# Performance work log

Measured on AMD Instinct MI355X. Metric: run time of the kernel, lower is better.

Reference implementation:

```python
import jax, jax.numpy as jnp
import numpy as np

A = 32      # num_agents (nodes per batch element)
B = 256     # batch size
T = 5       # temporal_window_size
H, C = 4, 64  # attention heads, hidden_dim per head
D = H * C   # feature_dim = 256
NEG_SLOPE = 0.2
LATENT = 128
NBS = 64    # num_belief_states
FIN = NBS + 16  # node_feat_dim = num_belief_states + action_dim


def _xavier(k, shape):
    std = (2.0 / (shape[0] + shape[-1])) ** 0.5
    return std * jax.random.normal(k, shape, dtype=jnp.float32)


def setup_inputs() -> dict:
    key = jax.random.key(0)
    ks = jax.random.split(key, 24)
    N = B * A
    # fully-connected directed graph (no self loops) inside each batch block
    ii, jj = np.meshgrid(np.arange(A), np.arange(A), indexing='ij')
    m = ii != jj
    off = (np.arange(B) * A)[:, None]
    src = (off + ii[m][None, :]).ravel()
    dst = (off + jj[m][None, :]).ravel()
    edge_index = jnp.asarray(np.stack([src, dst]), dtype=jnp.int32)  # [2, E]
    return dict(
        x_seq=jax.random.normal(ks[0], (T, N, FIN), dtype=jnp.float32),
        edge_index=edge_index,
        W1=_xavier(ks[1], (D, FIN)),
        att_src1=0.1 * jax.random.normal(ks[2], (H, C), dtype=jnp.float32),
        att_dst1=0.1 * jax.random.normal(ks[3], (H, C), dtype=jnp.float32),
        b1=jnp.zeros((D,), jnp.float32),
        W2=_xavier(ks[4], (D, D)),
        att_src2=0.1 * jax.random.normal(ks[5], (H, C), dtype=jnp.float32),
        att_dst2=0.1 * jax.random.normal(ks[6], (H, C), dtype=jnp.float32),
        b2=jnp.zeros((D,), jnp.float32),
        in_proj_w=_xavier(ks[7], (3 * D, D)),
        in_proj_b=jnp.zeros((3 * D,), jnp.float32),
        out_proj_w=_xavier(ks[8], (D, D)),
        out_proj_b=jnp.zeros((D,), jnp.float32),
        w_mean=_xavier(ks[9], (LATENT, D)),
        b_mean=jnp.zeros((LATENT,), jnp.float32),
        w_logvar=_xavier(ks[10], (LATENT, D)),
        b_logvar=jnp.zeros((LATENT,), jnp.float32),
        w_belief=_xavier(ks[11], (NBS, D)),
        b_belief=jnp.zeros((NBS,), jnp.float32),
    )


def _gat(x, src, dst, W, a_src, a_dst, bias, N):
    """PyG-style GATConv (concat heads, self loops already in src/dst, eval mode)."""
    h = (x @ W.T).reshape(N, H, C)                         # [N,H,C]
    e = (h * a_src).sum(-1)[src] + (h * a_dst).sum(-1)[dst]  # [E,H]
    e = jax.nn.leaky_relu(e, NEG_SLOPE)
    mx = jax.ops.segment_max(e, dst, num_segments=N)       # segment softmax over incoming edges
    ex = jnp.exp(e - mx[dst])
    denom = jax.ops.segment_sum(ex, dst, num_segments=N)
    alpha = ex / denom[dst]                                # [E,H]
    out = jax.ops.segment_sum(h[src] * alpha[:, :, None], dst, num_segments=N)
    return out.reshape(N, H * C) + bias


def reference(x_seq, edge_index, W1, att_src1, att_dst1, b1, W2, att_src2, att_dst2, b2,
              in_proj_w, in_proj_b, out_proj_w, out_proj_b,
              w_mean, b_mean, w_logvar, b_logvar, w_belief, b_belief):
    N = x_seq.shape[1]
    loops = jnp.arange(N, dtype=edge_index.dtype)          # GATConv adds self loops
    src = jnp.concatenate([edge_index[0], loops])
    dst = jnp.concatenate([edge_index[1], loops])
    ego = jnp.arange(0, N, A)                              # ego node of each batch element

    def step(_, x):
        hh = jax.nn.relu(_gat(x, src, dst, W1, att_src1, att_dst1, b1, N))
        hh = jax.nn.relu(_gat(hh, src, dst, W2, att_src2, att_dst2, b2, N))
        return None, hh[ego]                               # [B, D]

    _, outs = jax.lax.scan(step, None, x_seq)              # [T, B, D]
    seq = jnp.transpose(outs, (1, 0, 2))                   # [B, T, D]

    # nn.MultiheadAttention(batch_first=True), float additive mask of 1s (j<=i) / 0s (j>i)
    qkv = seq @ in_proj_w.T + in_proj_b
    q, k, v = jnp.split(qkv, 3, axis=-1)
    split = lambda t: t.reshape(B, T, H, D // H).transpose(0, 2, 1, 3)  # [B,H,T,dh]
    q, k, v = split(q), split(k), split(v)
    mask = (jnp.arange(T)[:, None] >= jnp.arange(T)[None, :]).astype(seq.dtype)
    scale = 1.0 / jnp.sqrt(jnp.asarray(D // H, seq.dtype))
    scores = jnp.einsum('bhqd,bhkd->bhqk', q, k) * scale + mask
    attn = jax.nn.softmax(scores, axis=-1)
    ctx = jnp.einsum('bhqk,bhkd->bhqd', attn, v).transpose(0, 2, 1, 3).reshape(B, T, D)
    attn_out = ctx @ out_proj_w.T + out_proj_b
    feat = attn_out[:, -1]                                 # [B, D]

    mean = feat @ w_mean.T + b_mean
    logvar = feat @ w_logvar.T + b_logvar
    belief = jax.nn.softmax(feat @ w_belief.T + b_belief, axis=-1)
    return mean, logvar, belief
```

## Files before the change

kernel.cpp:

```cpp
#include <hip/hip_runtime.h>

typedef _Float16 f16;
typedef __attribute__((ext_vector_type(2))) _Float16 f16x2;
typedef __attribute__((ext_vector_type(4))) _Float16 f16x4;
typedef __attribute__((ext_vector_type(8))) _Float16 f16x8;
typedef __attribute__((ext_vector_type(4))) float    f32x4;

#define NA 32
#define NB 256
#define NT 5
#define ND 256
#define NFIN 80
#define NLAT 128
#define NBEL 64
#define NEG 0.2f

#define W1K 96
#define XSTR 104
#define H1TSTR 40
#define HH1STR 264
#define ALSTR 40

#define OFF_HH1 0
#define OFF_H1T 16896
#define OFF_AL  37376
#define OFF_SD  47616
#define SMEM_SZ 48640

#define MFMA16(a,b,c) __builtin_amdgcn_mfma_f32_16x16x32_f16(a, b, c, 0, 0, 0)

#define WS_SEQ   0
#define WS_QKV   655360
#define WS_CTX   2621440
#define WS_W1F   2752512
#define WS_W2F   2801664
#define WS_IPW   2932736
#define WS_OPW   3325952
#define WS_HDW   3457024

__global__ void convert_w(const float* __restrict__ W1, const float* __restrict__ W2,
                          const float* __restrict__ ipw, const float* __restrict__ opw,
                          const float* __restrict__ wm, const float* __restrict__ wl,
                          const float* __restrict__ wb,
                          f16* __restrict__ W1f, f16* __restrict__ W2f,
                          f16* __restrict__ ipwf, f16* __restrict__ opwf,
                          f16* __restrict__ hdwf)
{
    const int i = blockIdx.x * 256 + threadIdx.x;
    if (i < 24576) {
        const int r = i / W1K, c = i - r * W1K;
        W1f[i] = (c < NFIN) ? (f16)W1[r * NFIN + c] : (f16)0.f;
    } else if (i < 90112) {
        const int j = i - 24576; W2f[j] = (f16)W2[j];
    } else if (i < 286720) {
        const int j = i - 90112; ipwf[j] = (f16)ipw[j];
    } else if (i < 352256) {
        const int j = i - 286720; opwf[j] = (f16)opw[j];
    } else if (i < 434176) {
        const int j = i - 352256;
        hdwf[j] = (f16)(j < 32768 ? wm[j] : (j < 65536 ? wl[j - 32768] : wb[j - 65536]));
    }
}

__global__ __launch_bounds__(256, 3)
void gnn_kernel(const float* __restrict__ x_seq,
                const f16*  __restrict__ W1f,
                const float* __restrict__ as1, const float* __restrict__ ad1,
                const float* __restrict__ b1,
                const f16*  __restrict__ W2f,
                const float* __restrict__ as2, const float* __restrict__ ad2,
                const float* __restrict__ b2,
                f16* __restrict__ seqf)
{
    __shared__ __align__(16) unsigned char smem[SMEM_SZ];
    f16*  Xs  = (f16*)(smem + OFF_HH1);
    f16*  hh1 = (f16*)(smem + OFF_HH1);
    f16*  h1T = (f16*)(smem + OFF_H1T);
    f16*  alp = (f16*)(smem + OFF_AL);
    float* sA = (float*)(smem + OFF_SD);
    float* dA = sA + 128;

    const int blk  = blockIdx.x;
    const int b    = blk / NT;
    const int t    = blk % NT;
    const int tid  = threadIdx.x;
    const int wv   = tid >> 6;
    const int lane = tid & 63;
    const int c    = lane & 15;
    const int g    = lane >> 4;
    const int n0   = wv * 64;

    const float* xg = x_seq + ((size_t)t * (NB * NA) + (size_t)b * NA) * NFIN;
    for (int idx = tid; idx < 640; idx += 256) {
        const int r = idx / 20, c4 = idx - r * 20;
        const float4 v = ((const float4*)xg)[idx];
        f16x4 h; h.x = (f16)v.x; h.y = (f16)v.y; h.z = (f16)v.z; h.w = (f16)v.w;
        *(f16x4*)(Xs + r * XSTR + c4 * 4) = h;
    }
    if (tid < 128) {
        const int r = tid >> 2, cc = tid & 3;
        f16x4 z; z.x = z.y = z.z = z.w = (f16)0.f;
        *(f16x4*)(Xs + r * XSTR + 80 + cc * 4) = z;
    }
    __syncthreads();

    f32x4 acc1[2][4];
#pragma unroll
    for (int m = 0; m < 2; ++m)
#pragma unroll
        for (int tn = 0; tn < 4; ++tn) acc1[m][tn] = (f32x4)0.f;

#pragma unroll
    for (int kt = 0; kt < 3; ++kt) {
        const int k0 = kt * 32 + 8 * g;
        f16x8 a0 = *(const f16x8*)(Xs + c * XSTR + k0);
        f16x8 a1 = *(const f16x8*)(Xs + (16 + c) * XSTR + k0);
#pragma unroll
        for (int tn = 0; tn < 4; ++tn) {
            f16x8 bw = *(const f16x8*)(W1f + (size_t)(n0 + 16 * tn + c) * W1K + k0);
            acc1[0][tn] = MFMA16(a0, bw, acc1[0][tn]);
            acc1[1][tn] = MFMA16(a1, bw, acc1[1][tn]);
        }
    }

    float asv[4], adv[4];
#pragma unroll
    for (int tn = 0; tn < 4; ++tn) {
        asv[tn] = as1[n0 + 16 * tn + c];
        adv[tn] = ad1[n0 + 16 * tn + c];
    }
    {
        float sv[2][4], dv[2][4];
#pragma unroll
        for (int m = 0; m < 2; ++m)
#pragma unroll
            for (int r = 0; r < 4; ++r) {
                float ps = 0.f, pd = 0.f;
#pragma unroll
                for (int tn = 0; tn < 4; ++tn) {
                    ps = fmaf(acc1[m][tn][r], asv[tn], ps);
                    pd = fmaf(acc1[m][tn][r], adv[tn], pd);
                }
#pragma unroll
                for (int off = 1; off < 16; off <<= 1) {
                    ps += __shfl_xor(ps, off, 64);
                    pd += __shfl_xor(pd, off, 64);
                }
                sv[m][r] = ps; dv[m][r] = pd;
            }
        if (c == 0) {
#pragma unroll
            for (int m = 0; m < 2; ++m)
#pragma unroll
                for (int r = 0; r < 4; ++r) {
                    sA[wv * 32 + 16 * m + 4 * g + r] = sv[m][r];
                    dA[wv * 32 + 16 * m + 4 * g + r] = dv[m][r];
                }
        }
    }

#pragma unroll
    for (int m = 0; m < 2; ++m)
#pragma unroll
        for (int tn = 0; tn < 4; ++tn) {
            f16x4 h;
            h.x = (f16)acc1[m][tn][0]; h.y = (f16)acc1[m][tn][1];
            h.z = (f16)acc1[m][tn][2]; h.w = (f16)acc1[m][tn][3];
            *(f16x4*)(h1T + (n0 + 16 * tn + c) * H1TSTR + 16 * m + 4 * g) = h;
        }

    if (lane < 32) {
        const float dd = dA[wv * 32 + lane];
        float e[32]; float mx = -1e30f;
#pragma unroll
        for (int i = 0; i < 32; ++i) {
            float v = sA[wv * 32 + i] + dd;
            v = (v >= 0.f) ? v : NEG * v;
            e[i] = v; mx = fmaxf(mx, v);
        }
        float den = 0.f;
#pragma unroll
        for (int i = 0; i < 32; ++i) { float p = __expf(e[i] - mx); e[i] = p; den += p; }
        const float rr = 1.f / den;
#pragma unroll
        for (int i2 = 0; i2 < 16; ++i2) {
            f16x2 p2; p2.x = (f16)(e[2 * i2] * rr); p2.y = (f16)(e[2 * i2 + 1] * rr);
            *(f16x2*)(alp + (wv * 32 + lane) * ALSTR + 2 * i2) = p2;
        }
    }

    f32x4 agg[2][4];
#pragma unroll
    for (int m = 0; m < 2; ++m)
#pragma unroll
        for (int tn = 0; tn < 4; ++tn) agg[m][tn] = (f32x4)0.f;
    {
        f16x8 aal0 = *(const f16x8*)(alp + (wv * 32 + c) * ALSTR + 8 * g);
        f16x8 aal1 = *(const f16x8*)(alp + (wv * 32 + 16 + c) * ALSTR + 8 * g);
#pragma unroll
        for (int tn = 0; tn < 4; ++tn) {
            f16x8 bh = *(const f16x8*)(h1T + (n0 + 16 * tn + c) * H1TSTR + 8 * g);
            agg[0][tn] = MFMA16(aal0, bh, agg[0][tn]);
            agg[1][tn] = MFMA16(aal1, bh, agg[1][tn]);
        }
    }

    __syncthreads();

    {
        float b1v[4];
#pragma unroll
        for (int tn = 0; tn < 4; ++tn) b1v[tn] = b1[n0 + 16 * tn + c];
#pragma unroll
        for (int m = 0; m < 2; ++m)
#pragma unroll
            for (int tn = 0; tn < 4; ++tn)
#pragma unroll
                for (int r = 0; r < 4; ++r) {
                    float val = fmaxf(agg[m][tn][r] + b1v[tn], 0.f);
                    hh1[(16 * m + 4 * g + r) * HH1STR + n0 + 16 * tn + c] = (f16)val;
                }
    }
    __syncthreads();

    f32x4 acc2[2][4];
#pragma unroll
    for (int m = 0; m < 2; ++m)
#pragma unroll
        for (int tn = 0; tn < 4; ++tn) acc2[m][tn] = (f32x4)0.f;

#pragma unroll
    for (int kt = 0; kt < 8; ++kt) {
        const int k0 = kt * 32 + 8 * g;
        f16x8 a0 = *(const f16x8*)(hh1 + c * HH1STR + k0);
        f16x8 a1 = *(const f16x8*)(hh1 + (16 + c) * HH1STR + k0);
#pragma unroll
        for (int tn = 0; tn < 4; ++tn) {
            f16x8 bw = *(const f16x8*)(W2f + (size_t)(n0 + 16 * tn + c) * ND + k0);
            acc2[0][tn] = MFMA16(a0, bw, acc2[0][tn]);
            acc2[1][tn] = MFMA16(a1, bw, acc2[1][tn]);
        }
    }

    float as2v[4], ad2v[4];
#pragma unroll
    for (int tn = 0; tn < 4; ++tn) {
        as2v[tn] = as2[n0 + 16 * tn + c];
        ad2v[tn] = ad2[n0 + 16 * tn + c];
    }
    {
        float sv[2][4];
#pragma unroll
        for (int m = 0; m < 2; ++m)
#pragma unroll
            for (int r = 0; r < 4; ++r) {
                float ps = 0.f;
#pragma unroll
                for (int tn = 0; tn < 4; ++tn) ps = fmaf(acc2[m][tn][r], as2v[tn], ps);
#pragma unroll
                for (int off = 1; off < 16; off <<= 1) ps += __shfl_xor(ps, off, 64);
                sv[m][r] = ps;
            }
        if (c == 0) {
#pragma unroll
            for (int m = 0; m < 2; ++m)
#pragma unroll
                for (int r = 0; r < 4; ++r)
                    sA[wv * 32 + 16 * m + 4 * g + r] = sv[m][r];
        }
    }
    float pd = 0.f;
#pragma unroll
    for (int tn = 0; tn < 4; ++tn) pd = fmaf(acc2[0][tn][0], ad2v[tn], pd);
#pragma unroll
    for (int off = 1; off < 16; off <<= 1) pd += __shfl_xor(pd, off, 64);
    const float d20 = __shfl(pd, 0, 64);

    {
        float mx = -1e30f;
#pragma unroll
        for (int i = 0; i < 32; ++i) {
            float v = sA[wv * 32 + i] + d20;
            v = (v >= 0.f) ? v : NEG * v;
            mx = fmaxf(mx, v);
        }
        float den = 0.f;
#pragma unroll
        for (int i = 0; i < 32; ++i) {
            float v = sA[wv * 32 + i] + d20;
            v = (v >= 0.f) ? v : NEG * v;
            den += __expf(v - mx);
        }
        float ev[2][4];
#pragma unroll
        for (int m = 0; m < 2; ++m)
#pragma unroll
            for (int r = 0; r < 4; ++r) {
                float v = sA[wv * 32 + 16 * m + 4 * g + r] + d20;
                v = (v >= 0.f) ? v : NEG * v;
                ev[m][r] = __expf(v - mx);
            }
        float b2v[4];
#pragma unroll
        for (int tn = 0; tn < 4; ++tn) b2v[tn] = b2[n0 + 16 * tn + c];
        const float rden = 1.f / den;
        f16* sq = seqf + ((size_t)b * NT + t) * ND;
#pragma unroll
        for (int tn = 0; tn < 4; ++tn) {
            float o = 0.f;
#pragma unroll
            for (int m = 0; m < 2; ++m)
#pragma unroll
                for (int r = 0; r < 4; ++r) o = fmaf(ev[m][r], acc2[m][tn][r], o);
            o += __shfl_xor(o, 16, 64);
            o += __shfl_xor(o, 32, 64);
            if (g == 0) sq[n0 + 16 * tn + c] = (f16)fmaxf(o * rden + b2v[tn], 0.f);
        }
    }
}

#define QASTR 264
__global__ __launch_bounds__(256, 4)
void qkv_kernel(const f16* __restrict__ seqf, const f16* __restrict__ ipwf,
                const float* __restrict__ ipb, f16* __restrict__ qkv)
{
    __shared__ __align__(16) f16 As[64 * QASTR];

    const int bx  = blockIdx.x;
    const int m0  = (bx % 20) * 64;
    const int n0  = (bx / 20) * 128;
    const int tid = threadIdx.x;
    const int wv  = tid >> 6;
    const int lane = tid & 63;
    const int c   = lane & 15;
    const int g   = lane >> 4;
    const int mb  = (wv >> 1) * 32;
    const int nb  = n0 + (wv & 1) * 64;

    for (int idx = tid; idx < 2048; idx += 256) {
        const int r = idx >> 5, c8 = idx & 31;
        *(f16x8*)(As + r * QASTR + c8 * 8) =
            *(const f16x8*)(seqf + (size_t)(m0 + r) * ND + c8 * 8);
    }
    __syncthreads();

    f32x4 acc[2][4];
#pragma unroll
    for (int m = 0; m < 2; ++m)
#pragma unroll
        for (int tn = 0; tn < 4; ++tn) acc[m][tn] = (f32x4)0.f;

#pragma unroll
    for (int kt = 0; kt < 8; ++kt) {
        const int k0 = kt * 32 + 8 * g;
        f16x8 a0 = *(const f16x8*)(As + (mb + c) * QASTR + k0);
        f16x8 a1 = *(const f16x8*)(As + (mb + 16 + c) * QASTR + k0);
#pragma unroll
        for (int tn = 0; tn < 4; ++tn) {
            f16x8 bw = *(const f16x8*)(ipwf + (size_t)(nb + 16 * tn + c) * ND + k0);
            acc[0][tn] = MFMA16(a0, bw, acc[0][tn]);
            acc[1][tn] = MFMA16(a1, bw, acc[1][tn]);
        }
    }

    float bias[4];
#pragma unroll
    for (int tn = 0; tn < 4; ++tn) bias[tn] = ipb[nb + 16 * tn + c];
#pragma unroll
    for (int m = 0; m < 2; ++m)
#pragma unroll
        for (int tn = 0; tn < 4; ++tn)
#pragma unroll
            for (int r = 0; r < 4; ++r) {
                const int row = m0 + mb + 16 * m + 4 * g + r;
                qkv[(size_t)row * 768 + nb + 16 * tn + c] =
                    (f16)(acc[m][tn][r] + bias[tn]);
            }
}

__global__ __launch_bounds__(256, 4)
void attn_kernel(const f16* __restrict__ qkv, f16* __restrict__ ctx)
{
    const int b    = blockIdx.x;
    const int wv   = threadIdx.x >> 6;
    const int lane = threadIdx.x & 63;
    const int ch   = wv * 64 + lane;

    const float q = (float)qkv[(size_t)(b * 5 + 4) * 768 + ch];
    float kv[NT], vv[NT];
#pragma unroll
    for (int t = 0; t < NT; ++t) {
        kv[t] = (float)qkv[(size_t)(b * 5 + t) * 768 + 256 + ch];
        vv[t] = (float)qkv[(size_t)(b * 5 + t) * 768 + 512 + ch];
    }
    float sc[NT];
#pragma unroll
    for (int t = 0; t < NT; ++t) {
        float p = q * kv[t];
#pragma unroll
        for (int off = 32; off > 0; off >>= 1) p += __shfl_xor(p, off, 64);
        sc[t] = p * 0.125f;
    }
    float m = sc[0];
#pragma unroll
    for (int t = 1; t < NT; ++t) m = fmaxf(m, sc[t]);
    float den = 0.f, o = 0.f;
#pragma unroll
    for (int t = 0; t < NT; ++t) {
        float p = __expf(sc[t] - m);
        den += p;
        o = fmaf(p, vv[t], o);
    }
    ctx[(size_t)b * ND + ch] = (f16)(o / den);
}

#define FASTR 264
__global__ __launch_bounds__(256, 2)
void final_kernel(const f16* __restrict__ ctx,
                  const f16* __restrict__ opwf, const float* __restrict__ opb,
                  const f16* __restrict__ hdwf,
                  const float* __restrict__ bm, const float* __restrict__ blv,
                  const float* __restrict__ bb,
                  float* __restrict__ out)
{
    __shared__ __align__(16) f16 As[32 * FASTR];
    __shared__ __align__(16) f16 Fs[32 * FASTR];
    __shared__ __align__(16) float Bs[32 * 68];

    const int m0   = blockIdx.x * 32;
    const int tid  = threadIdx.x;
    const int wv   = tid >> 6;
    const int lane = tid & 63;
    const int c    = lane & 15;
    const int g    = lane >> 4;

    for (int idx = tid; idx < 1024; idx += 256) {
        const int r = idx >> 5, c8 = idx & 31;
        *(f16x8*)(As + r * FASTR + c8 * 8) =
            *(const f16x8*)(ctx + (size_t)(m0 + r) * ND + c8 * 8);
    }
    __syncthreads();

    {
        f32x4 acc[2][4];
#pragma unroll
        for (int m = 0; m < 2; ++m)
#pragma unroll
            for (int tn = 0; tn < 4; ++tn) acc[m][tn] = (f32x4)0.f;
#pragma unroll
        for (int kt = 0; kt < 8; ++kt) {
            const int k0 = kt * 32 + 8 * g;
            f16x8 a0 = *(const f16x8*)(As + c * FASTR + k0);
            f16x8 a1 = *(const f16x8*)(As + (16 + c) * FASTR + k0);
#pragma unroll
            for (int tn = 0; tn < 4; ++tn) {
                f16x8 bw = *(const f16x8*)(opwf + (size_t)(wv * 64 + 16 * tn + c) * ND + k0);
                acc[0][tn] = MFMA16(a0, bw, acc[0][tn]);
                acc[1][tn] = MFMA16(a1, bw, acc[1][tn]);
            }
        }
        float bias[4];
#pragma unroll
        for (int tn = 0; tn < 4; ++tn) bias[tn] = opb[wv * 64 + 16 * tn + c];
#pragma unroll
        for (int m = 0; m < 2; ++m)
#pragma unroll
            for (int tn = 0; tn < 4; ++tn)
#pragma unroll
                for (int r = 0; r < 4; ++r)
                    Fs[(16 * m + 4 * g + r) * FASTR + wv * 64 + 16 * tn + c] =
                        (f16)(acc[m][tn][r] + bias[tn]);
    }
    __syncthreads();

    {
        f32x4 acc[2][5];
#pragma unroll
        for (int m = 0; m < 2; ++m)
#pragma unroll
            for (int fi = 0; fi < 5; ++fi) acc[m][fi] = (f32x4)0.f;
#pragma unroll
        for (int kt = 0; kt < 8; ++kt) {
            const int k0 = kt * 32 + 8 * g;
            f16x8 a0 = *(const f16x8*)(Fs + c * FASTR + k0);
            f16x8 a1 = *(const f16x8*)(Fs + (16 + c) * FASTR + k0);
#pragma unroll
            for (int fi = 0; fi < 5; ++fi) {
                const int nf = 5 * wv + fi;
                f16x8 bw = *(const f16x8*)(hdwf + (size_t)(16 * nf + c) * ND + k0);
                acc[0][fi] = MFMA16(a0, bw, acc[0][fi]);
                acc[1][fi] = MFMA16(a1, bw, acc[1][fi]);
            }
        }
#pragma unroll
        for (int fi = 0; fi < 5; ++fi) {
            const int ocol = 16 * (5 * wv + fi) + c;
            float bias;
            if (ocol < 128)       bias = bm[ocol];
            else if (ocol < 256)  bias = blv[ocol - 128];
            else                  bias = bb[ocol - 256];
#pragma unroll
            for (int m = 0; m < 2; ++m)
#pragma unroll
                for (int r = 0; r < 4; ++r) {
                    const int row = 16 * m + 4 * g + r;
                    const float v = acc[m][fi][r] + bias;
                    if (ocol < 128)
                        out[(size_t)(m0 + row) * NLAT + ocol] = v;
                    else if (ocol < 256)
                        out[(size_t)NB * NLAT + (size_t)(m0 + row) * NLAT + (ocol - 128)] = v;
                    else
                        Bs[row * 68 + (ocol - 256)] = v;
                }
        }
    }
    __syncthreads();

    for (int rr = 0; rr < 8; ++rr) {
        const int row = wv * 8 + rr;
        float x = Bs[row * 68 + lane];
        float mm = x;
#pragma unroll
        for (int off = 32; off > 0; off >>= 1) mm = fmaxf(mm, __shfl_xor(mm, off, 64));
        float p = __expf(x - mm);
        float dd = p;
#pragma unroll
        for (int off = 32; off > 0; off >>= 1) dd += __shfl_xor(dd, off, 64);
        out[(size_t)2 * NB * NLAT + (size_t)(m0 + row) * NBEL + lane] = p / dd;
    }
}

extern "C" void kernel_launch(void* const* d_in, const int* in_sizes, int n_in,
                              void* d_out, int out_size, void* d_ws, size_t ws_size,
                              hipStream_t stream)
{
    (void)in_sizes; (void)n_in; (void)out_size; (void)ws_size;
    const float* x_seq = (const float*)d_in[0];
    const float* W1  = (const float*)d_in[2];
    const float* as1 = (const float*)d_in[3];
    const float* ad1 = (const float*)d_in[4];
    const float* b1  = (const float*)d_in[5];
    const float* W2  = (const float*)d_in[6];
    const float* as2 = (const float*)d_in[7];
    const float* ad2 = (const float*)d_in[8];
    const float* b2  = (const float*)d_in[9];
    const float* ipw = (const float*)d_in[10];
    const float* ipb = (const float*)d_in[11];
    const float* opw = (const float*)d_in[12];
    const float* opb = (const float*)d_in[13];
    const float* wm  = (const float*)d_in[14];
    const float* bm  = (const float*)d_in[15];
    const float* wl  = (const float*)d_in[16];
    const float* bl  = (const float*)d_in[17];
    const float* wb  = (const float*)d_in[18];
    const float* bb  = (const float*)d_in[19];

    char* ws = (char*)d_ws;
    f16* seqf = (f16*)(ws + WS_SEQ);
    f16* qkv  = (f16*)(ws + WS_QKV);
    f16* ctx  = (f16*)(ws + WS_CTX);
    f16* W1f  = (f16*)(ws + WS_W1F);
    f16* W2f  = (f16*)(ws + WS_W2F);
    f16* ipwf = (f16*)(ws + WS_IPW);
    f16* opwf = (f16*)(ws + WS_OPW);
    f16* hdwf = (f16*)(ws + WS_HDW);
    float* out = (float*)d_out;

    hipLaunchKernelGGL(convert_w, dim3(1696), dim3(256), 0, stream,
                       W1, W2, ipw, opw, wm, wl, wb, W1f, W2f, ipwf, opwf, hdwf);
    hipLaunchKernelGGL(gnn_kernel, dim3(NB * NT), dim3(256), 0, stream,
                       x_seq, W1f, as1, ad1, b1, W2f, as2, ad2, b2, seqf);
    hipLaunchKernelGGL(qkv_kernel, dim3(120), dim3(256), 0, stream,
                       seqf, ipwf, ipb, qkv);
    hipLaunchKernelGGL(attn_kernel, dim3(NB), dim3(256), 0, stream, qkv, ctx);
    hipLaunchKernelGGL(final_kernel, dim3(8), dim3(256), 0, stream,
                       ctx, opwf, opb, hdwf, bm, bl, bb, out);
}
```

Before: 69.97 us.

## Fold attention vectors into weights and compute GAT scores with extra MFMA

Precomputes att_src·W and att_dst·W (per head) as small fp16 weight matrices in the conversion kernel, so per-node source/destination attention logits come from one extra MFMA column tile instead of post-GEMM FMA plus cross-lane shuffle reductions. The softmax over 32 neighbours is split across both half-waves with a shuffle combine, and shared memory is shrunk by overlaying the alpha buffer, allowing launch bounds of 4 blocks per CU. Risks include reduced precision from computing logits from fp16-rounded folded weights and register pressure at the higher occupancy target.

```diff
diff --git a/kernel.cpp b/kernel.cpp
--- a/kernel.cpp
+++ b/kernel.cpp
@@ -21,11 +21,12 @@
 #define HH1STR 264
 #define ALSTR 40
 
+#define OFF_XS  0
+#define OFF_ALP 6656
 #define OFF_HH1 0
 #define OFF_H1T 16896
-#define OFF_AL  37376
-#define OFF_SD  47616
-#define SMEM_SZ 48640
+#define OFF_SD  37376
+#define SMEM_SZ 38400
 
 #define MFMA16(a,b,c) __builtin_amdgcn_mfma_f32_16x16x32_f16(a, b, c, 0, 0, 0)
 
@@ -37,14 +38,19 @@
 #define WS_IPW   2932736
 #define WS_OPW   3325952
 #define WS_HDW   3457024
+#define WS_WSD1  3620864
+#define WS_WSD2  3623936
 
 __global__ void convert_w(const float* __restrict__ W1, const float* __restrict__ W2,
                           const float* __restrict__ ipw, const float* __restrict__ opw,
                           const float* __restrict__ wm, const float* __restrict__ wl,
                           const float* __restrict__ wb,
+                          const float* __restrict__ as1, const float* __restrict__ ad1,
+                          const float* __restrict__ as2, const float* __restrict__ ad2,
                           f16* __restrict__ W1f, f16* __restrict__ W2f,
                           f16* __restrict__ ipwf, f16* __restrict__ opwf,
-                          f16* __restrict__ hdwf)
+                          f16* __restrict__ hdwf,
+                          f16* __restrict__ wsd1f, f16* __restrict__ wsd2f)
 {
     const int i = blockIdx.x * 256 + threadIdx.x;
     if (i < 24576) {
@@ -59,24 +65,44 @@
     } else if (i < 434176) {
         const int j = i - 352256;
         hdwf[j] = (f16)(j < 32768 ? wm[j] : (j < 65536 ? wl[j - 32768] : wb[j - 65536]));
+    } else if (i < 435712) {
+        const int j = i - 434176;
+        const int o = j / 96, f = j - o * 96;
+        float v = 0.f;
+        if (o < 8 && f < NFIN) {
+            const int h = o & 3;
+            const float* av = (o < 4) ? as1 : ad1;
+            for (int cc = 0; cc < 64; ++cc)
+                v = fmaf(av[h * 64 + cc], W1[(h * 64 + cc) * NFIN + f], v);
+        }
+        wsd1f[j] = (f16)v;
+    } else if (i < 439808) {
+        const int j = i - 435712;
+        const int o = j >> 8, k = j & 255;
+        float v = 0.f;
+        if (o < 8) {
+            const int h = o & 3;
+            const float* av = (o < 4) ? as2 : ad2;
+            for (int cc = 0; cc < 64; ++cc)
+                v = fmaf(av[h * 64 + cc], W2[(h * 64 + cc) * ND + k], v);
+        }
+        wsd2f[j] = (f16)v;
     }
 }
 
-__global__ __launch_bounds__(256, 3)
+__global__ __launch_bounds__(256, 4)
 void gnn_kernel(const float* __restrict__ x_seq,
-                const f16*  __restrict__ W1f,
-                const float* __restrict__ as1, const float* __restrict__ ad1,
+                const f16*  __restrict__ W1f,  const f16* __restrict__ wsd1f,
                 const float* __restrict__ b1,
-                const f16*  __restrict__ W2f,
-                const float* __restrict__ as2, const float* __restrict__ ad2,
+                const f16*  __restrict__ W2f,  const f16* __restrict__ wsd2f,
                 const float* __restrict__ b2,
                 f16* __restrict__ seqf)
 {
     __shared__ __align__(16) unsigned char smem[SMEM_SZ];
-    f16*  Xs  = (f16*)(smem + OFF_HH1);
+    f16*  Xs  = (f16*)(smem + OFF_XS);
     f16*  hh1 = (f16*)(smem + OFF_HH1);
+    f16*  alp = (f16*)(smem + OFF_ALP);
     f16*  h1T = (f16*)(smem + OFF_H1T);
-    f16*  alp = (f16*)(smem + OFF_AL);
     float* sA = (float*)(smem + OFF_SD);
     float* dA = sA + 128;
 
@@ -104,17 +130,21 @@
     }
     __syncthreads();
 
-    f32x4 acc1[2][4];
-#pragma unroll
-    for (int m = 0; m < 2; ++m)
+    f32x4 acc1[2][4]; f32x4 accS[2];
+#pragma unroll
+    for (int m = 0; m < 2; ++m) {
+        accS[m] = (f32x4)0.f;
 #pragma unroll
         for (int tn = 0; tn < 4; ++tn) acc1[m][tn] = (f32x4)0.f;
-
+    }
 #pragma unroll
     for (int kt = 0; kt < 3; ++kt) {
         const int k0 = kt * 32 + 8 * g;
         f16x8 a0 = *(const f16x8*)(Xs + c * XSTR + k0);
         f16x8 a1 = *(const f16x8*)(Xs + (16 + c) * XSTR + k0);
+        f16x8 bs = *(const f16x8*)(wsd1f + c * W1K + k0);
+        accS[0] = MFMA16(a0, bs, accS[0]);
+        accS[1] = MFMA16(a1, bs, accS[1]);
 #pragma unroll
         for (int tn = 0; tn < 4; ++tn) {
             f16x8 bw = *(const f16x8*)(W1f + (size_t)(n0 + 16 * tn + c) * W1K + k0);
@@ -123,40 +153,18 @@
         }
     }
 
-    float asv[4], adv[4];
-#pragma unroll
-    for (int tn = 0; tn < 4; ++tn) {
-        asv[tn] = as1[n0 + 16 * tn + c];
-        adv[tn] = ad1[n0 + 16 * tn + c];
-    }
-    {
-        float sv[2][4], dv[2][4];
-#pragma unroll
-        for (int m = 0; m < 2; ++m)
-#pragma unroll
-            for (int r = 0; r < 4; ++r) {
-                float ps = 0.f, pd = 0.f;
-#pragma unroll
-                for (int tn = 0; tn < 4; ++tn) {
-                    ps = fmaf(acc1[m][tn][r], asv[tn], ps);
-                    pd = fmaf(acc1[m][tn][r], adv[tn], pd);
-                }
-#pragma unroll
-                for (int off = 1; off < 16; off <<= 1) {
-                    ps += __shfl_xor(ps, off, 64);
-                    pd += __shfl_xor(pd, off, 64);
-                }
-                sv[m][r] = ps; dv[m][r] = pd;
-            }
-        if (c == 0) {
-#pragma unroll
-            for (int m = 0; m < 2; ++m)
-#pragma unroll
-                for (int r = 0; r < 4; ++r) {
-                    sA[wv * 32 + 16 * m + 4 * g + r] = sv[m][r];
-                    dA[wv * 32 + 16 * m + 4 * g + r] = dv[m][r];
-                }
-        }
+    if (c == wv) {
+#pragma unroll
+        for (int m = 0; m < 2; ++m)
+#pragma unroll
+            for (int r = 0; r < 4; ++r)
+                sA[wv * 32 + 16 * m + 4 * g + r] = accS[m][r];
+    } else if (c == wv + 4) {
+#pragma unroll
+        for (int m = 0; m < 2; ++m)
+#pragma unroll
+            for (int r = 0; r < 4; ++r)
+                dA[wv * 32 + 16 * m + 4 * g + r] = accS[m][r];
     }
 
 #pragma unroll
@@ -169,23 +177,29 @@
             *(f16x4*)(h1T + (n0 + 16 * tn + c) * H1TSTR + 16 * m + 4 * g) = h;
         }
 
-    if (lane < 32) {
-        const float dd = dA[wv * 32 + lane];
-        float e[32]; float mx = -1e30f;
-#pragma unroll
-        for (int i = 0; i < 32; ++i) {
-            float v = sA[wv * 32 + i] + dd;
+    {
+        const int j = lane & 31;
+        const int half = lane >> 5;
+        const float dd = dA[wv * 32 + j];
+        const float* sbase = sA + wv * 32 + 16 * half;
+        float e[16]; float mx = -1e30f;
+#pragma unroll
+        for (int i = 0; i < 16; ++i) {
+            float v = sbase[i] + dd;
             v = (v >= 0.f) ? v : NEG * v;
             e[i] = v; mx = fmaxf(mx, v);
         }
+        mx = fmaxf(mx, __shfl_xor(mx, 32, 64));
         float den = 0.f;
 #pragma unroll
-        for (int i = 0; i < 32; ++i) { float p = __expf(e[i] - mx); e[i] = p; den += p; }
+        for (int i = 0; i < 16; ++i) { float p = __expf(e[i] - mx); e[i] = p; den += p; }
+        den += __shfl_xor(den, 32, 64);
         const float rr = 1.f / den;
-#pragma unroll
-        for (int i2 = 0; i2 < 16; ++i2) {
+        f16* arow = alp + (wv * 32 + j) * ALSTR + 16 * half;
+#pragma unroll
+        for (int i2 = 0; i2 < 8; ++i2) {
             f16x2 p2; p2.x = (f16)(e[2 * i2] * rr); p2.y = (f16)(e[2 * i2 + 1] * rr);
-            *(f16x2*)(alp + (wv * 32 + lane) * ALSTR + 2 * i2) = p2;
+            *(f16x2*)(arow + 2 * i2) = p2;
         }
     }
 
@@ -223,17 +237,21 @@
     }
     __syncthreads();
 
-    f32x4 acc2[2][4];
-#pragma unroll
-    for (int m = 0; m < 2; ++m)
+    f32x4 acc2[2][4]; f32x4 accS2[2];
+#pragma unroll
+    for (int m = 0; m < 2; ++m) {
+        accS2[m] = (f32x4)0.f;
 #pragma unroll
         for (int tn = 0; tn < 4; ++tn) acc2[m][tn] = (f32x4)0.f;
-
+    }
 #pragma unroll
     for (int kt = 0; kt < 8; ++kt) {
         const int k0 = kt * 32 + 8 * g;
         f16x8 a0 = *(const f16x8*)(hh1 + c * HH1STR + k0);
         f16x8 a1 = *(const f16x8*)(hh1 + (16 + c) * HH1STR + k0);
+        f16x8 bs = *(const f16x8*)(wsd2f + c * ND + k0);
+        accS2[0] = MFMA16(a0, bs, accS2[0]);
+        accS2[1] = MFMA16(a1, bs, accS2[1]);
 #pragma unroll
         for (int tn = 0; tn < 4; ++tn) {
             f16x8 bw = *(const f16x8*)(W2f + (size_t)(n0 + 16 * tn + c) * ND + k0);
@@ -242,39 +260,16 @@
         }
     }
 
-    float as2v[4], ad2v[4];
-#pragma unroll
-    for (int tn = 0; tn < 4; ++tn) {
-        as2v[tn] = as2[n0 + 16 * tn + c];
-        ad2v[tn] = ad2[n0 + 16 * tn + c];
-    }
-    {
-        float sv[2][4];
-#pragma unroll
-        for (int m = 0; m < 2; ++m)
-#pragma unroll
-            for (int r = 0; r < 4; ++r) {
-                float ps = 0.f;
-#pragma unroll
-                for (int tn = 0; tn < 4; ++tn) ps = fmaf(acc2[m][tn][r], as2v[tn], ps);
-#pragma unroll
-                for (int off = 1; off < 16; off <<= 1) ps += __shfl_xor(ps, off, 64);
-                sv[m][r] = ps;
-            }
-        if (c == 0) {
-#pragma unroll
-            for (int m = 0; m < 2; ++m)
-#pragma unroll
-                for (int r = 0; r < 4; ++r)
-                    sA[wv * 32 + 16 * m + 4 * g + r] = sv[m][r];
-        }
-    }
-    float pd = 0.f;
-#pragma unroll
-    for (int tn = 0; tn < 4; ++tn) pd = fmaf(acc2[0][tn][0], ad2v[tn], pd);
-#pragma unroll
-    for (int off = 1; off < 16; off <<= 1) pd += __shfl_xor(pd, off, 64);
-    const float d20 = __shfl(pd, 0, 64);
+    if (c == wv) {
+#pragma unroll
+        for (int m = 0; m < 2; ++m)
+#pragma unroll
+            for (int r = 0; r < 4; ++r)
+                sA[wv * 32 + 16 * m + 4 * g + r] = accS2[m][r];
+    }
+    if (c == wv + 4 && g == 0) dA[wv * 32] = accS2[0][0];
+
+    const float d20 = dA[wv * 32];
 
     {
         float mx = -1e30f;
@@ -556,20 +551,23 @@
     const float* bb  = (const float*)d_in[19];
 
     char* ws = (char*)d_ws;
-    f16* seqf = (f16*)(ws + WS_SEQ);
-    f16* qkv  = (f16*)(ws + WS_QKV);
-    f16* ctx  = (f16*)(ws + WS_CTX);
-    f16* W1f  = (f16*)(ws + WS_W1F);
-    f16* W2f  = (f16*)(ws + WS_W2F);
-    f16* ipwf = (f16*)(ws + WS_IPW);
-    f16* opwf = (f16*)(ws + WS_OPW);
-    f16* hdwf = (f16*)(ws + WS_HDW);
+    f16* seqf  = (f16*)(ws + WS_SEQ);
+    f16* qkv   = (f16*)(ws + WS_QKV);
+    f16* ctx   = (f16*)(ws + WS_CTX);
+    f16* W1f   = (f16*)(ws + WS_W1F);
+    f16* W2f   = (f16*)(ws + WS_W2F);
+    f16* ipwf  = (f16*)(ws + WS_IPW);
+    f16* opwf  = (f16*)(ws + WS_OPW);
+    f16* hdwf  = (f16*)(ws + WS_HDW);
+    f16* wsd1f = (f16*)(ws + WS_WSD1);
+    f16* wsd2f = (f16*)(ws + WS_WSD2);
     float* out = (float*)d_out;
 
-    hipLaunchKernelGGL(convert_w, dim3(1696), dim3(256), 0, stream,
-                       W1, W2, ipw, opw, wm, wl, wb, W1f, W2f, ipwf, opwf, hdwf);
+    hipLaunchKernelGGL(convert_w, dim3(1718), dim3(256), 0, stream,
+                       W1, W2, ipw, opw, wm, wl, wb, as1, ad1, as2, ad2,
+                       W1f, W2f, ipwf, opwf, hdwf, wsd1f, wsd2f);
     hipLaunchKernelGGL(gnn_kernel, dim3(NB * NT), dim3(256), 0, stream,
-                       x_seq, W1f, as1, ad1, b1, W2f, as2, ad2, b2, seqf);
+                       x_seq, W1f, wsd1f, b1, W2f, wsd2f, b2, seqf);
     hipLaunchKernelGGL(qkv_kernel, dim3(120), dim3(256), 0, stream,
                        seqf, ipwf, ipb, qkv);
     hipLaunchKernelGGL(attn_kernel, dim3(NB), dim3(256), 0, stream, qkv, ctx);
```

Result: no change. 71.33 us (+1.9%).
